# Optimization experiments

Hardware: AMD Instinct MI355X
Metric: run time of the kernel (lower is better)

Reference implementation:

```python
import jax, jax.numpy as jnp
import numpy as np

FP8_MAX = 448.0  # e4m3 max
SCALE_MARGIN = 0.8


def _fp8_quant_dequant(t, scale):
    # scaled value is <= 448*0.8 by construction, so no saturation/overflow
    q = (t / scale).astype(jnp.float8_e4m3fn)
    return q.astype(jnp.float32) * scale


def setup_inputs() -> dict:
    key = jax.random.key(0)
    k1, k2 = jax.random.split(key)
    B, S, D_IN, D_OUT = 4, 2048, 2048, 2048
    x = jax.random.normal(k1, (B, S, D_IN), dtype=jnp.float32)
    weight = jax.random.normal(k2, (D_OUT, D_IN), dtype=jnp.float32)
    bias = jnp.zeros((D_OUT,), dtype=jnp.float32)
    return {"x": x, "weight": weight, "bias": bias}


def reference(x, weight, bias):
    # Shared FP8ScalingManager: amax history = [amax_x] for x, then [amax_x, amax_w] for w.
    amax_x = jnp.max(jnp.abs(x))
    amax_w = jnp.max(jnp.abs(weight))
    x_scale = amax_x / (FP8_MAX * SCALE_MARGIN)
    w_scale = jnp.maximum(amax_x, amax_w) / (FP8_MAX * SCALE_MARGIN)  # history max
    x_scale = jax.lax.stop_gradient(x_scale)  # .item() detaches in torch
    w_scale = jax.lax.stop_gradient(w_scale)
    # quantize to fp8 e4m3, dequantize, scaled matmul (math of torch._scaled_mm)
    x_dq = _fp8_quant_dequant(x, x_scale)      # [B,S,Din]
    w_dq = _fp8_quant_dequant(weight, w_scale)  # [Dout,Din]
    out = jnp.einsum('bsd,od->bso', x_dq, w_dq)  # [B,S,Dout]
    return out + bias
```

## Files before the change

kernel.cpp:

```cpp
#include <hip/hip_runtime.h>
#include <stdint.h>

typedef float v4f __attribute__((ext_vector_type(4)));
typedef int v8i __attribute__((ext_vector_type(8)));

#define FP8_DENOM 358.4f


__device__ __forceinline__ unsigned pack4_fp8(float a, float b, float c, float d) {
  int v = 0;
  v = __builtin_amdgcn_cvt_pk_fp8_f32(a, b, v, false);
  v = __builtin_amdgcn_cvt_pk_fp8_f32(c, d, v, true);
  return (unsigned)v;
}

__device__ __forceinline__ void gload_lds16(const void* g, void* l) {
  __builtin_amdgcn_global_load_lds(
      (const __attribute__((address_space(1))) uint32_t*)(uintptr_t)g,
      (__attribute__((address_space(3))) uint32_t*)(uint32_t)(uintptr_t)l,
      16, 0, 0);
}


__global__ void __launch_bounds__(256) amax_part(const float4* __restrict__ x,
                                                 const float4* __restrict__ w,
                                                 float* __restrict__ part) {
  const int b = blockIdx.x, t = threadIdx.x;
  const float4* p = (b < 1024) ? x : w;
  const long base = (long)((b < 1024) ? b : (b - 1024)) * 4096;
  float m0 = 0.f, m1 = 0.f, m2 = 0.f, m3 = 0.f;
#pragma unroll
  for (int j = 0; j < 4; ++j) {
    float4 v0 = p[base + (j * 4 + 0) * 256 + t];
    float4 v1 = p[base + (j * 4 + 1) * 256 + t];
    float4 v2 = p[base + (j * 4 + 2) * 256 + t];
    float4 v3 = p[base + (j * 4 + 3) * 256 + t];
    m0 = fmaxf(m0, fmaxf(fmaxf(fabsf(v0.x), fabsf(v0.y)), fmaxf(fabsf(v0.z), fabsf(v0.w))));
    m1 = fmaxf(m1, fmaxf(fmaxf(fabsf(v1.x), fabsf(v1.y)), fmaxf(fabsf(v1.z), fabsf(v1.w))));
    m2 = fmaxf(m2, fmaxf(fmaxf(fabsf(v2.x), fabsf(v2.y)), fmaxf(fabsf(v2.z), fabsf(v2.w))));
    m3 = fmaxf(m3, fmaxf(fmaxf(fabsf(v3.x), fabsf(v3.y)), fmaxf(fabsf(v3.z), fabsf(v3.w))));
  }
  float m = fmaxf(fmaxf(m0, m1), fmaxf(m2, m3));
#pragma unroll
  for (int off = 32; off > 0; off >>= 1)
    m = fmaxf(m, __shfl_down(m, off, 64));
  __shared__ float red[4];
  const int lane = t & 63, wvid = t >> 6;
  if (lane == 0) red[wvid] = m;
  __syncthreads();
  if (t == 0) part[b] = fmaxf(fmaxf(red[0], red[1]), fmaxf(red[2], red[3]));
}


__global__ void __launch_bounds__(256) scale_reduce(const float* __restrict__ part,
                                                    unsigned* __restrict__ amax) {
  const int t = threadIdx.x;
  float mx = fmaxf(fmaxf(part[t], part[t + 256]), fmaxf(part[t + 512], part[t + 768]));
  float mw = part[1024 + t];
#pragma unroll
  for (int off = 32; off > 0; off >>= 1) {
    mx = fmaxf(mx, __shfl_down(mx, off, 64));
    mw = fmaxf(mw, __shfl_down(mw, off, 64));
  }
  __shared__ float rx[4], rw[4];
  const int lane = t & 63, wvid = t >> 6;
  if (lane == 0) { rx[wvid] = mx; rw[wvid] = mw; }
  __syncthreads();
  if (t == 0) {
    const float ax = fmaxf(fmaxf(rx[0], rx[1]), fmaxf(rx[2], rx[3]));
    const float aw = fmaxf(fmaxf(rw[0], rw[1]), fmaxf(rw[2], rw[3]));
    const float sx = ax / FP8_DENOM;
    const float sw = fmaxf(ax, aw) / FP8_DENOM;
    amax[0] = __float_as_uint(ax);
    amax[1] = __float_as_uint(aw);
    amax[2] = __float_as_uint(1.0f / sx);
    amax[3] = __float_as_uint(1.0f / sw);
    amax[4] = __float_as_uint(sx * sw);
  }
}


__global__ void quant2_kernel(const float4* __restrict__ x, uint4* __restrict__ xq, int nx16,
                              const float4* __restrict__ w, uint4* __restrict__ wq, int nw16,
                              int xblocks, const unsigned* __restrict__ amax) {
  const int isw = ((int)blockIdx.x >= xblocks) ? 1 : 0;
  const float rs = __uint_as_float(amax[2 + isw]);
  const float4* in = isw ? w : x;
  uint4* outq = isw ? wq : xq;
  const int n16 = isw ? nw16 : nx16;
  const int b0 = isw ? ((int)blockIdx.x - xblocks) : (int)blockIdx.x;
  const int nb = isw ? ((int)gridDim.x - xblocks) : xblocks;
  const long stride = (long)nb * blockDim.x;
  for (long i = (long)b0 * blockDim.x + threadIdx.x; i < n16; i += stride) {
    float4 v0 = in[4 * i + 0], v1 = in[4 * i + 1], v2 = in[4 * i + 2], v3 = in[4 * i + 3];
    uint4 r;
    r.x = pack4_fp8(v0.x * rs, v0.y * rs, v0.z * rs, v0.w * rs);
    r.y = pack4_fp8(v1.x * rs, v1.y * rs, v1.z * rs, v1.w * rs);
    r.z = pack4_fp8(v2.x * rs, v2.y * rs, v2.z * rs, v2.w * rs);
    r.w = pack4_fp8(v3.x * rs, v3.y * rs, v3.z * rs, v3.w * rs);
    outq[i] = r;
  }
}


__global__ void __launch_bounds__(256) gemm_mx(
    const uint8_t* __restrict__ Aq, const uint8_t* __restrict__ Bq,
    const float* __restrict__ bias, float* __restrict__ out,
    const unsigned* __restrict__ amax) {
  constexpr int K = 2048, N = 2048, BK = 128, ITERS = K / BK;
  __shared__ alignas(16) uint8_t sA[2][128 * BK];
  __shared__ alignas(16) uint8_t sB[2][128 * BK];

  const int tid = threadIdx.x;
  const int lane = tid & 63;
  const int wid = tid >> 6;
  const int wy = wid >> 1, wx = wid & 1;
  const long tileM = (long)blockIdx.y * 128;
  const long tileN = (long)blockIdx.x * 128;

  v4f acc[4][4];
#pragma unroll
  for (int i = 0; i < 4; ++i)
#pragma unroll
    for (int j = 0; j < 4; ++j) acc[i][j] = (v4f)(0.f);

  const int srow = tid >> 3;
  const int schunk = (tid & 7) ^ (srow & 7);
  const uint8_t* gA = Aq + (tileM + srow) * K + schunk * 16;
  const uint8_t* gB = Bq + (tileN + srow) * K + schunk * 16;

  const int q = lane >> 4;
  const int mrow = lane & 15;

  int aoff[4][2], boff[4][2];
#pragma unroll
  for (int i = 0; i < 4; ++i) {
    const int rA = wy * 64 + i * 16 + mrow, swA = rA & 7;
    aoff[i][0] = rA * 128 + 16 * ((2 * q) ^ swA);
    aoff[i][1] = rA * 128 + 16 * ((2 * q + 1) ^ swA);
    const int rB = wx * 64 + i * 16 + mrow, swB = rB & 7;
    boff[i][0] = rB * 128 + 16 * ((2 * q) ^ swB);
    boff[i][1] = rB * 128 + 16 * ((2 * q + 1) ^ swB);
  }

  auto stage = [&](int buf, int k0) {
#pragma unroll
    for (int s = 0; s < 4; ++s) {
      gload_lds16(gA + (long)s * 32 * K + k0, &sA[buf][s * 4096 + tid * 16]);
      gload_lds16(gB + (long)s * 32 * K + k0, &sB[buf][s * 4096 + tid * 16]);
    }
  };

  stage(0, 0);
  for (int it = 0; it < ITERS; ++it) {
    __syncthreads();
    if (it + 1 < ITERS) stage((it + 1) & 1, (it + 1) * BK);

    const uint8_t* bufA = sA[it & 1];
    const uint8_t* bufB = sB[it & 1];
    union Frag { v8i v; uint4 h[2]; };
    Frag a[4], b[4];
#pragma unroll
    for (int i = 0; i < 4; ++i) {
      a[i].h[0] = *(const uint4*)(bufA + aoff[i][0]);
      a[i].h[1] = *(const uint4*)(bufA + aoff[i][1]);
      b[i].h[0] = *(const uint4*)(bufB + boff[i][0]);
      b[i].h[1] = *(const uint4*)(bufB + boff[i][1]);
    }
#pragma unroll
    for (int i = 0; i < 4; ++i)
#pragma unroll
      for (int j = 0; j < 4; ++j)
        acc[i][j] = __builtin_amdgcn_mfma_scale_f32_16x16x128_f8f6f4(
            a[i].v, b[j].v, acc[i][j],  0,  0,
             0, 0x7F7F7F7F,  0, 0x7F7F7F7F);
  }

  const float scale = __uint_as_float(amax[4]);
#pragma unroll
  for (int j = 0; j < 4; ++j) {
    const long col = tileN + wx * 64 + j * 16 + mrow;
    const float bv = bias[col];
#pragma unroll
    for (int i = 0; i < 4; ++i) {
      const long row = tileM + wy * 64 + i * 16 + q * 4;
#pragma unroll
      for (int r = 0; r < 4; ++r)
        out[(row + r) * N + col] = acc[i][j][r] * scale + bv;
    }
  }
}


extern "C" void kernel_launch(void* const* d_in, const int* in_sizes, int n_in,
                              void* d_out, int out_size, void* d_ws, size_t ws_size,
                              hipStream_t stream) {
  const float* x = (const float*)d_in[0];
  const float* w = (const float*)d_in[1];
  const float* bias = (const float*)d_in[2];
  float* out = (float*)d_out;

  const int M = 8192, N = 2048, K = 2048;
  const long nx = (long)M * K, nw = (long)N * K;

  unsigned* amax = (unsigned*)d_ws;
  float* part = (float*)((uint8_t*)d_ws + 256);
  uint8_t* xq = (uint8_t*)d_ws + 8192;
  uint8_t* wq = xq + nx;

  amax_part<<<1280, 256, 0, stream>>>((const float4*)x, (const float4*)w, part);
  scale_reduce<<<1, 256, 0, stream>>>(part, amax);
  quant2_kernel<<<5120, 256, 0, stream>>>((const float4*)x, (uint4*)xq, (int)(nx / 16),
                                          (const float4*)w, (uint4*)wq, (int)(nw / 16),
                                          4096, amax);
  gemm_mx<<<dim3(N / 128, M / 128), 256, 0, stream>>>(xq, wq, bias, out, amax);
}
```

Before: 175.3 us.

## Fuse amax reduction and fp8 quantization into one persistent kernel with grid barrier

New measurement: 249.8 us. 1.43x slower.

```diff
diff --git a/kernel.cpp b/kernel.cpp
--- a/kernel.cpp
+++ b/kernel.cpp
@@ -21,42 +21,28 @@
       16, 0, 0);
 }
 
-
-__global__ void __launch_bounds__(256) amax_part(const float4* __restrict__ x,
-                                                 const float4* __restrict__ w,
-                                                 float* __restrict__ part) {
-  const int b = blockIdx.x, t = threadIdx.x;
-  const float4* p = (b < 1024) ? x : w;
-  const long base = (long)((b < 1024) ? b : (b - 1024)) * 4096;
-  float m0 = 0.f, m1 = 0.f, m2 = 0.f, m3 = 0.f;
-#pragma unroll
-  for (int j = 0; j < 4; ++j) {
-    float4 v0 = p[base + (j * 4 + 0) * 256 + t];
-    float4 v1 = p[base + (j * 4 + 1) * 256 + t];
-    float4 v2 = p[base + (j * 4 + 2) * 256 + t];
-    float4 v3 = p[base + (j * 4 + 3) * 256 + t];
-    m0 = fmaxf(m0, fmaxf(fmaxf(fabsf(v0.x), fabsf(v0.y)), fmaxf(fabsf(v0.z), fabsf(v0.w))));
-    m1 = fmaxf(m1, fmaxf(fmaxf(fabsf(v1.x), fabsf(v1.y)), fmaxf(fabsf(v1.z), fabsf(v1.w))));
-    m2 = fmaxf(m2, fmaxf(fmaxf(fabsf(v2.x), fabsf(v2.y)), fmaxf(fabsf(v2.z), fabsf(v2.w))));
-    m3 = fmaxf(m3, fmaxf(fmaxf(fabsf(v3.x), fabsf(v3.y)), fmaxf(fabsf(v3.z), fabsf(v3.w))));
-  }
-  float m = fmaxf(fmaxf(m0, m1), fmaxf(m2, m3));
-#pragma unroll
-  for (int off = 32; off > 0; off >>= 1)
-    m = fmaxf(m, __shfl_down(m, off, 64));
-  __shared__ float red[4];
-  const int lane = t & 63, wvid = t >> 6;
-  if (lane == 0) red[wvid] = m;
-  __syncthreads();
-  if (t == 0) part[b] = fmaxf(fmaxf(red[0], red[1]), fmaxf(red[2], red[3]));
+__device__ __forceinline__ float amax4(float m, float4 v) {
+  return fmaxf(m, fmaxf(fmaxf(fabsf(v.x), fabsf(v.y)), fmaxf(fabsf(v.z), fabsf(v.w))));
 }
 
 
-__global__ void __launch_bounds__(256) scale_reduce(const float* __restrict__ part,
-                                                    unsigned* __restrict__ amax) {
+__global__ void __launch_bounds__(256) amax_quant(
+    const float4* __restrict__ x, unsigned* __restrict__ xq,
+    const float4* __restrict__ w, unsigned* __restrict__ wq,
+    unsigned* __restrict__ sync) {
+  constexpr int NX4 = 4194304;
+  constexpr int NW4 = 1048576;
+  constexpr int GRID = 512;
+  constexpr int GSIZE = GRID * 256;
   const int t = threadIdx.x;
-  float mx = fmaxf(fmaxf(part[t], part[t + 256]), fmaxf(part[t + 512], part[t + 768]));
-  float mw = part[1024 + t];
+  const int gtid = (int)blockIdx.x * 256 + t;
+
+  float mx = 0.f, mw = 0.f;
+#pragma unroll 8
+  for (int j = 0; j < NX4 / GSIZE; ++j) mx = amax4(mx, x[gtid + j * GSIZE]);
+#pragma unroll 8
+  for (int j = 0; j < NW4 / GSIZE; ++j) mw = amax4(mw, w[gtid + j * GSIZE]);
+
 #pragma unroll
   for (int off = 32; off > 0; off >>= 1) {
     mx = fmaxf(mx, __shfl_down(mx, off, 64));
@@ -67,38 +53,31 @@
   if (lane == 0) { rx[wvid] = mx; rw[wvid] = mw; }
   __syncthreads();
   if (t == 0) {
-    const float ax = fmaxf(fmaxf(rx[0], rx[1]), fmaxf(rx[2], rx[3]));
-    const float aw = fmaxf(fmaxf(rw[0], rw[1]), fmaxf(rw[2], rw[3]));
-    const float sx = ax / FP8_DENOM;
-    const float sw = fmaxf(ax, aw) / FP8_DENOM;
-    amax[0] = __float_as_uint(ax);
-    amax[1] = __float_as_uint(aw);
-    amax[2] = __float_as_uint(1.0f / sx);
-    amax[3] = __float_as_uint(1.0f / sw);
-    amax[4] = __float_as_uint(sx * sw);
+    atomicMax(sync + 0, __float_as_uint(fmaxf(fmaxf(rx[0], rx[1]), fmaxf(rx[2], rx[3]))));
+    atomicMax(sync + 1, __float_as_uint(fmaxf(fmaxf(rw[0], rw[1]), fmaxf(rw[2], rw[3]))));
+    __threadfence();
+    __hip_atomic_fetch_add(sync + 2, 1u, __ATOMIC_ACQ_REL, __HIP_MEMORY_SCOPE_AGENT);
+    while (__hip_atomic_load(sync + 2, __ATOMIC_ACQUIRE, __HIP_MEMORY_SCOPE_AGENT) < GRID)
+      __builtin_amdgcn_s_sleep(2);
   }
-}
+  __syncthreads();
 
+  const float ax = __uint_as_float(
+      __hip_atomic_load(sync + 0, __ATOMIC_ACQUIRE, __HIP_MEMORY_SCOPE_AGENT));
+  const float aw = __uint_as_float(
+      __hip_atomic_load(sync + 1, __ATOMIC_ACQUIRE, __HIP_MEMORY_SCOPE_AGENT));
+  const float rsx = 1.0f / (ax / FP8_DENOM);
+  const float rsw = 1.0f / (fmaxf(ax, aw) / FP8_DENOM);
 
-__global__ void quant2_kernel(const float4* __restrict__ x, uint4* __restrict__ xq, int nx16,
-                              const float4* __restrict__ w, uint4* __restrict__ wq, int nw16,
-                              int xblocks, const unsigned* __restrict__ amax) {
-  const int isw = ((int)blockIdx.x >= xblocks) ? 1 : 0;
-  const float rs = __uint_as_float(amax[2 + isw]);
-  const float4* in = isw ? w : x;
-  uint4* outq = isw ? wq : xq;
-  const int n16 = isw ? nw16 : nx16;
-  const int b0 = isw ? ((int)blockIdx.x - xblocks) : (int)blockIdx.x;
-  const int nb = isw ? ((int)gridDim.x - xblocks) : xblocks;
-  const long stride = (long)nb * blockDim.x;
-  for (long i = (long)b0 * blockDim.x + threadIdx.x; i < n16; i += stride) {
-    float4 v0 = in[4 * i + 0], v1 = in[4 * i + 1], v2 = in[4 * i + 2], v3 = in[4 * i + 3];
-    uint4 r;
-    r.x = pack4_fp8(v0.x * rs, v0.y * rs, v0.z * rs, v0.w * rs);
-    r.y = pack4_fp8(v1.x * rs, v1.y * rs, v1.z * rs, v1.w * rs);
-    r.z = pack4_fp8(v2.x * rs, v2.y * rs, v2.z * rs, v2.w * rs);
-    r.w = pack4_fp8(v3.x * rs, v3.y * rs, v3.z * rs, v3.w * rs);
-    outq[i] = r;
+#pragma unroll 4
+  for (int j = 0; j < NX4 / GSIZE; ++j) {
+    float4 v = x[gtid + j * GSIZE];
+    xq[gtid + j * GSIZE] = pack4_fp8(v.x * rsx, v.y * rsx, v.z * rsx, v.w * rsx);
+  }
+#pragma unroll 4
+  for (int j = 0; j < NW4 / GSIZE; ++j) {
+    float4 v = w[gtid + j * GSIZE];
+    wq[gtid + j * GSIZE] = pack4_fp8(v.x * rsw, v.y * rsw, v.z * rsw, v.w * rsw);
   }
 }
 
@@ -176,7 +155,9 @@
              0, 0x7F7F7F7F,  0, 0x7F7F7F7F);
   }
 
-  const float scale = __uint_as_float(amax[4]);
+  const float ax = __uint_as_float(amax[0]);
+  const float aw = __uint_as_float(amax[1]);
+  const float scale = (ax / FP8_DENOM) * (fmaxf(ax, aw) / FP8_DENOM);
 #pragma unroll
   for (int j = 0; j < 4; ++j) {
     const long col = tileN + wx * 64 + j * 16 + mrow;
@@ -201,17 +182,15 @@
   float* out = (float*)d_out;
 
   const int M = 8192, N = 2048, K = 2048;
-  const long nx = (long)M * K, nw = (long)N * K;
+  const long nx = (long)M * K;
 
-  unsigned* amax = (unsigned*)d_ws;
-  float* part = (float*)((uint8_t*)d_ws + 256);
+  unsigned* syncw = (unsigned*)d_ws;
   uint8_t* xq = (uint8_t*)d_ws + 8192;
   uint8_t* wq = xq + nx;
 
-  amax_part<<<1280, 256, 0, stream>>>((const float4*)x, (const float4*)w, part);
-  scale_reduce<<<1, 256, 0, stream>>>(part, amax);
-  quant2_kernel<<<5120, 256, 0, stream>>>((const float4*)x, (uint4*)xq, (int)(nx / 16),
-                                          (const float4*)w, (uint4*)wq, (int)(nw / 16),
-                                          4096, amax);
-  gemm_mx<<<dim3(N / 128, M / 128), 256, 0, stream>>>(xq, wq, bias, out, amax);
+  hipMemsetAsync(syncw, 0, 16, stream);
+
+  amax_quant<<<512, 256, 0, stream>>>((const float4*)x, (unsigned*)xq,
+                                      (const float4*)w, (unsigned*)wq, syncw);
+  gemm_mx<<<dim3(N / 128, M / 128), 256, 0, stream>>>(xq, wq, bias, out, syncw);
 }
```
